# Performance work log

Measured on AMD Instinct MI355X. Metric: run time of the kernel, lower is better.

The kernel has to match this reference:

```python
import jax, jax.numpy as jnp
import numpy as np

PARTITIONS = [1, 2, 4, 8, 16, 32]
FORECAST = 720
D_MODEL = 256
B, C = 64, 64


def len_of_split_into_k_parts(L, k):
    avg, rem = L // k, L % k
    return [avg + (1 if i < rem else 0) for i in range(k)]


def setup_inputs() -> dict:
    key = jax.random.key(0)
    keys = jax.random.split(key, 1 + 2 * len(PARTITIONS))
    T = sum(PARTITIONS)
    inp = {"x": jax.random.normal(keys[0], (B, C, T, D_MODEL), dtype=jnp.float32)}
    for i, k in enumerate(PARTITIONS):
        max_len = max(len_of_split_into_k_parts(FORECAST, k))
        bound = 1.0 / np.sqrt(D_MODEL)
        inp[f"W{i}"] = jax.random.uniform(keys[1 + 2 * i], (max_len, D_MODEL), minval=-bound, maxval=bound, dtype=jnp.float32)
        inp[f"b{i}"] = jax.random.uniform(keys[2 + 2 * i], (max_len,), minval=-bound, maxval=bound, dtype=jnp.float32)
    return inp


def _forward(x, Ws, bs):
    idx = 0
    total = None
    for i, k in enumerate(PARTITIONS):
        split = len_of_split_into_k_parts(FORECAST, k)
        x_r = x[..., idx:idx + k, :]                      # [B, C, k, d]
        idx += k
        proj = jnp.einsum('bctd,md->bctm', x_r, Ws[i]) + bs[i]  # [B, C, k, max_len]
        # ragged slice+concat: token s contributes its first split[s] positions
        tok = np.repeat(np.arange(k), split)              # [f] static indices
        pos = np.concatenate([np.arange(s) for s in split])  # [f]
        res = proj[..., tok, pos]                         # [B, C, f]
        total = res if total is None else total + res
    return jnp.swapaxes(total, -1, -2)                    # [B, f, C]


def reference(x, W0, b0, W1, b1, W2, b2, W3, b3, W4, b4, W5, b5):
    Ws = [W0, W1, W2, W3, W4, W5]
    bs = [b0, b1, b2, b3, b4, b5]
    return _forward(x, Ws, bs)
```

## Files before the change

### kernel.cpp

```cpp
#include <hip/hip_runtime.h>
#include <stdint.h>


#define FDIM 720
#define DDIM 256
#define TDIM 63
#define NSUBTOT 299
#define TAB_BYTES ((size_t)NSUBTOT * 8 * 1024)
#define OUTELEMS ((size_t)64 * FDIM * 64)
#define NCHUNK 80
#define CH 6

typedef __attribute__((ext_vector_type(8))) short short8;
typedef __attribute__((ext_vector_type(4))) float f32x4;

__device__ __forceinline__ uint32_t pkru(float a, float b) {
    uint32_t ua = __builtin_bit_cast(uint32_t, a) + 0x8000u;
    uint32_t ub = __builtin_bit_cast(uint32_t, b) + 0x8000u;
    return __builtin_amdgcn_perm(ub, ua, 0x07060302u);
}
__device__ __forceinline__ short8 loadpack(const float* p) {
    float4 v0 = *(const float4*)p;
    float4 v1 = *(const float4*)(p + 4);
    uint4 u;
    u.x = pkru(v0.x, v0.y);
    u.y = pkru(v0.z, v0.w);
    u.z = pkru(v1.x, v1.y);
    u.w = pkru(v1.z, v1.w);
    return __builtin_bit_cast(short8, u);
}

__device__ __forceinline__ void atomAddF(float* p, float v) {
    unsafeAtomicAdd(p, v);
}

__device__ __forceinline__ void jpos(int i, int f, int& j, int& pos) {
    switch (i) {
        case 0: j = 0;       pos = f;            break;
        case 1: j = f / 360; pos = f - 360 * j;  break;
        case 2: j = f / 180; pos = f - 180 * j;  break;
        case 3: j = f / 90;  pos = f - 90 * j;   break;
        case 4: j = f / 45;  pos = f - 45 * j;   break;
        default:
            if (f < 368) { j = f / 23;  pos = f - 23 * j; }
            else { int g = f - 368; int q = g / 22; j = 16 + q; pos = g - 22 * q; }
            break;
    }
}

__device__ __forceinline__ void tok_params(int tok, int& len, int& ns,
                                           int& start, int& tabsub) {
    if (tok < 1)       { len = 720; ns = 45; start = 0;
                         tabsub = 0; }
    else if (tok < 3)  { int j = tok - 1;  len = 360; ns = 23; start = 360 * j;
                         tabsub = 45 + j * 23; }
    else if (tok < 7)  { int j = tok - 3;  len = 180; ns = 12; start = 180 * j;
                         tabsub = 91 + j * 12; }
    else if (tok < 15) { int j = tok - 7;  len = 90;  ns = 6;  start = 90 * j;
                         tabsub = 139 + j * 6; }
    else if (tok < 31) { int j = tok - 15; len = 45;  ns = 3;  start = 45 * j;
                         tabsub = 187 + j * 3; }
    else               { int j = tok - 31;
                         len = (j < 16) ? 23 : 22;
                         start = (j < 16) ? 23 * j : 368 + 22 * (j - 16);
                         ns = 2; tabsub = 235 + j * 2; }
}

__device__ __forceinline__ void chunk_params(int cid, int& tok, int& s0) {
    if (cid < 8)       { tok = 0;               s0 = CH * cid; }
    else if (cid < 16) { int q = cid - 8;  tok = 1 + (q >> 2); s0 = CH * (q & 3); }
    else if (cid < 24) { int q = cid - 16; tok = 3 + (q >> 1); s0 = CH * (q & 1); }
    else if (cid < 32) { tok = 7 + (cid - 24);  s0 = 0; }
    else if (cid < 48) { tok = 15 + (cid - 32); s0 = 0; }
    else               { tok = 31 + (cid - 48); s0 = 0; }
}

__global__ __launch_bounds__(256) void olrs_prep(
    const float* __restrict__ W0, const float* __restrict__ W1,
    const float* __restrict__ W2, const float* __restrict__ W3,
    const float* __restrict__ W4, const float* __restrict__ W5,
    char* __restrict__ ws)
{
    const int gid  = blockIdx.x * 256 + threadIdx.x;
    const int lane = gid & 63;
    const int fid  = gid >> 6;
    if (fid >= NSUBTOT * 8) return;
    const int ks = fid & 7;
    const int g  = fid >> 3;

    int len; const float* W;
    int s;
    if (g < 45)       { W = W0; len = 720; s = g; }
    else if (g < 91)  { int g2 = g - 45;  W = W1; len = 360; s = g2 % 23; }
    else if (g < 139) { int g2 = g - 91;  W = W2; len = 180; s = g2 % 12; }
    else if (g < 187) { int g2 = g - 139; W = W3; len = 90;  s = g2 % 6; }
    else if (g < 235) { int g2 = g - 187; W = W4; len = 45;  s = g2 % 3; }
    else              { int g2 = g - 235; W = W5; int j = g2 >> 1;
                        len = (j < 16) ? 23 : 22; s = g2 & 1; }

    const int m15  = lane & 15;
    const int koct = lane >> 4;
    const int pos  = s * 16 + m15;
    uint4 u = {0u, 0u, 0u, 0u};
    if (pos < len) {
        const float* src = W + (size_t)pos * DDIM + ks * 32 + koct * 8;
        float4 v0 = *(const float4*)src;
        float4 v1 = *(const float4*)(src + 4);
        u.x = pkru(v0.x, v0.y);
        u.y = pkru(v0.z, v0.w);
        u.z = pkru(v1.x, v1.y);
        u.w = pkru(v1.z, v1.w);
    }
    *(uint4*)(ws + (size_t)fid * 1024 + lane * 16) = u;
}

__global__ __launch_bounds__(256) void olrs_init(
    const float* __restrict__ b0, const float* __restrict__ b1,
    const float* __restrict__ b2, const float* __restrict__ b3,
    const float* __restrict__ b4, const float* __restrict__ b5,
    float* __restrict__ out)
{
    const size_t base = ((size_t)blockIdx.x * 256 + threadIdx.x) * 4;
    if (base >= OUTELEMS) return;
    const int f = (int)((base >> 6) % FDIM);
    int j, p;
    float s = b0[f];
    jpos(1, f, j, p); s += b1[p];
    jpos(2, f, j, p); s += b2[p];
    jpos(3, f, j, p); s += b3[p];
    jpos(4, f, j, p); s += b4[p];
    jpos(5, f, j, p); s += b5[p];
    float4 o = {s, s, s, s};
    *(float4*)(out + base) = o;
}

__global__ __launch_bounds__(256) void olrs_main_at(
    const float* __restrict__ x,
    const char* __restrict__ ws,
    float* __restrict__ out)
{
    const int wid   = blockIdx.x * 4 + (threadIdx.x >> 6);
    const int lane  = threadIdx.x & 63;
    const int cid   = wid >> 7;
    const int ntile = wid & 127;
    const int b     = ntile >> 1;
    const int c0    = (ntile & 1) << 5;
    const int m15   = lane & 15;
    const int koct  = lane >> 4;

    int tok, s0;
    chunk_params(cid, tok, s0);
    int len, ns, start, tabsub;
    tok_params(tok, len, ns, start, tabsub);
    const int send = (s0 + CH < ns) ? (s0 + CH) : ns;

    const float* xpl = x + (((size_t)(b * 64 + c0 + m15)) * TDIM + tok) * DDIM;
    const float* xph = xpl + (size_t)16 * TDIM * DDIM;
    short8 xl[8], xh[8];
    #pragma unroll
    for (int ks = 0; ks < 8; ks++)
        xl[ks] = loadpack(xpl + ks * 32 + koct * 8);
    #pragma unroll
    for (int ks = 0; ks < 8; ks++)
        xh[ks] = loadpack(xph + ks * 32 + koct * 8);

    const char* tab = ws + (size_t)tabsub * 8192 + lane * 16;
    float* obl = out + ((size_t)b * FDIM + start) * 64 + c0 + m15;
    float* obh = obl + 16;

    short8 wA[8], wB[8];

    auto loadW = [&](short8* w, int s) {
        const char* t = tab + (size_t)s * 8192;
        #pragma unroll
        for (int ks = 0; ks < 8; ks++)
            w[ks] = *(const short8*)(t + ks * 1024);
    };
    auto compute = [&](const short8* w, int s) {
        f32x4 al0 = {0.f, 0.f, 0.f, 0.f}, al1 = {0.f, 0.f, 0.f, 0.f};
        f32x4 ah0 = {0.f, 0.f, 0.f, 0.f}, ah1 = {0.f, 0.f, 0.f, 0.f};
        #pragma unroll
        for (int ks = 0; ks < 8; ks += 2) {
            al0 = __builtin_amdgcn_mfma_f32_16x16x32_bf16(w[ks],     xl[ks],     al0, 0, 0, 0);
            ah0 = __builtin_amdgcn_mfma_f32_16x16x32_bf16(w[ks],     xh[ks],     ah0, 0, 0, 0);
            al1 = __builtin_amdgcn_mfma_f32_16x16x32_bf16(w[ks + 1], xl[ks + 1], al1, 0, 0, 0);
            ah1 = __builtin_amdgcn_mfma_f32_16x16x32_bf16(w[ks + 1], xh[ks + 1], ah1, 0, 0, 0);
        }
        const int fl0 = s * 16 + koct * 4;
        #pragma unroll
        for (int rg = 0; rg < 4; rg++) {
            const int fl = fl0 + rg;
            if (fl < len) {
                atomAddF(obl + (size_t)fl * 64, al0[rg] + al1[rg]);
                atomAddF(obh + (size_t)fl * 64, ah0[rg] + ah1[rg]);
            }
        }
    };

    int s = s0;
    loadW(wA, s);
    for (;;) {
        if (s + 1 < send) loadW(wB, s + 1);
        compute(wA, s);
        if (++s >= send) break;
        if (s + 1 < send) loadW(wA, s + 1);
        compute(wB, s);
        if (++s >= send) break;
    }
}

__device__ __forceinline__ int startf(int i, int j) {
    switch (i) {
        case 0: return 0;
        case 1: return 360 * j;
        case 2: return 180 * j;
        case 3: return 90 * j;
        case 4: return 45 * j;
        default: return (j < 16) ? 23 * j : 368 + 22 * (j - 16);
    }
}

__global__ __launch_bounds__(256) void olrs_fb(
    const float* __restrict__ x,
    const float* __restrict__ W0, const float* __restrict__ b0,
    const float* __restrict__ W1, const float* __restrict__ b1,
    const float* __restrict__ W2, const float* __restrict__ b2,
    const float* __restrict__ W3, const float* __restrict__ b3,
    const float* __restrict__ W4, const float* __restrict__ b4,
    const float* __restrict__ W5, const float* __restrict__ b5,
    float* __restrict__ out)
{
    const float* Wp[6] = {W0, W1, W2, W3, W4, W5};
    const float* bp[6] = {b0, b1, b2, b3, b4, b5};
    const int TB[6] = {0, 1, 3, 7, 15, 31};

    const int wid  = blockIdx.x * 4 + (threadIdx.x >> 6);
    const int lane = threadIdx.x & 63;
    const int ft   = wid % 45;
    const int bc   = wid / 45;
    const int b    = bc >> 2;
    const int c0   = (bc & 3) << 4;
    const int f0   = ft << 4;
    const int m15  = lane & 15;
    const int koct = lane >> 4;
    const size_t xrow = (size_t)(b * 64 + c0 + m15) * TDIM;

    f32x4 acc = {0.f, 0.f, 0.f, 0.f};
    #pragma unroll
    for (int i = 0; i < 6; i++) {
        int jlo, plo, jhi, phi;
        jpos(i, f0, jlo, plo);
        jpos(i, f0 + 15, jhi, phi);
        const bool cross = (jhi > jlo);
        const int fb = cross ? (startf(i, jhi) - f0) : 16;
        const float* xlo = x + (xrow + TB[i] + jlo) * DDIM;
        const float* xhi = x + (xrow + TB[i] + jhi) * DDIM;
        int jw, pw;
        jpos(i, f0 + m15, jw, pw);
        const float* wsrc = Wp[i] + (size_t)pw * DDIM;
        #pragma unroll
        for (int ks = 0; ks < 8; ks++) {
            const int d0 = ks * 32 + koct * 8;
            short8 a = loadpack(wsrc + d0);
            short8 blo = loadpack(xlo + d0);
            if (!cross) {
                acc = __builtin_amdgcn_mfma_f32_16x16x32_bf16(a, blo, acc, 0, 0, 0);
            } else {
                short8 bhi = loadpack(xhi + d0);
                short8 z;
                #pragma unroll
                for (int q = 0; q < 8; q++) z[q] = 0;
                short8 alo = (m15 < fb) ? a : z;
                short8 ahi = (m15 < fb) ? z : a;
                acc = __builtin_amdgcn_mfma_f32_16x16x32_bf16(alo, blo, acc, 0, 0, 0);
                acc = __builtin_amdgcn_mfma_f32_16x16x32_bf16(ahi, bhi, acc, 0, 0, 0);
            }
        }
    }
    #pragma unroll
    for (int rg = 0; rg < 4; rg++) {
        const int f = f0 + koct * 4 + rg;
        float bias = 0.f;
        #pragma unroll
        for (int i = 0; i < 6; i++) {
            int j, pos;
            jpos(i, f, j, pos);
            bias += bp[i][pos];
        }
        out[((size_t)b * FDIM + f) * 64 + c0 + m15] = acc[rg] + bias;
    }
}

extern "C" void kernel_launch(void* const* d_in, const int* in_sizes, int n_in,
                              void* d_out, int out_size, void* d_ws, size_t ws_size,
                              hipStream_t stream) {
    (void)in_sizes; (void)n_in; (void)out_size;

    const float* x  = (const float*)d_in[0];
    const float* W0 = (const float*)d_in[1];
    const float* b0 = (const float*)d_in[2];
    const float* W1 = (const float*)d_in[3];
    const float* b1 = (const float*)d_in[4];
    const float* W2 = (const float*)d_in[5];
    const float* b2 = (const float*)d_in[6];
    const float* W3 = (const float*)d_in[7];
    const float* b3 = (const float*)d_in[8];
    const float* W4 = (const float*)d_in[9];
    const float* b4 = (const float*)d_in[10];
    const float* W5 = (const float*)d_in[11];
    const float* b5 = (const float*)d_in[12];
    float* out = (float*)d_out;

    if (ws_size >= TAB_BYTES) {
        char* ws = (char*)d_ws;
        olrs_prep<<<dim3(NSUBTOT * 8 * 64 / 256), dim3(256), 0, stream>>>(
            W0, W1, W2, W3, W4, W5, ws);
        olrs_init<<<dim3((unsigned)(OUTELEMS / 4 / 256)), dim3(256), 0, stream>>>(
            b0, b1, b2, b3, b4, b5, out);
        olrs_main_at<<<dim3(NCHUNK * 128 / 4), dim3(256), 0, stream>>>(x, ws, out);
    } else {
        olrs_fb<<<dim3(45 * 256), dim3(256), 0, stream>>>(
            x, W0, b0, W1, b1, W2, b2, W3, b3, W4, b4, W5, b5, out);
    }
}
```

Before: 91.66 us.

## Merge prep/init kernels and share bf16 x tiles through LDS across waves

Fuses the weight-table packing kernel and the bias-initialisation kernel into one launch, removing a kernel launch and its gap. The main kernel now assigns the four waves of a block to chunks of the same token (or paired tokens), so the block loads and converts each x tile to bf16 once, stages it in LDS in MFMA fragment order, and every wave reads it from there. Before, each wave re-read and re-converted the same x data from global memory. This adds a block barrier and 32 KB of LDS per block, which may reduce occupancy.

```diff
diff --git a/kernel.cpp b/kernel.cpp
--- a/kernel.cpp
+++ b/kernel.cpp
@@ -8,8 +8,7 @@
 #define NSUBTOT 299
 #define TAB_BYTES ((size_t)NSUBTOT * 8 * 1024)
 #define OUTELEMS ((size_t)64 * FDIM * 64)
-#define NCHUNK 80
-#define CH 6
+#define NPREPTHR (NSUBTOT * 8 * 64)
 
 typedef __attribute__((ext_vector_type(8))) short short8;
 typedef __attribute__((ext_vector_type(4))) float f32x4;
@@ -66,103 +65,133 @@
                          ns = 2; tabsub = 235 + j * 2; }
 }
 
-__device__ __forceinline__ void chunk_params(int cid, int& tok, int& s0) {
-    if (cid < 8)       { tok = 0;               s0 = CH * cid; }
-    else if (cid < 16) { int q = cid - 8;  tok = 1 + (q >> 2); s0 = CH * (q & 3); }
-    else if (cid < 24) { int q = cid - 16; tok = 3 + (q >> 1); s0 = CH * (q & 1); }
-    else if (cid < 32) { tok = 7 + (cid - 24);  s0 = 0; }
-    else if (cid < 48) { tok = 15 + (cid - 32); s0 = 0; }
-    else               { tok = 31 + (cid - 48); s0 = 0; }
-}
-
-__global__ __launch_bounds__(256) void olrs_prep(
+__global__ __launch_bounds__(256) void olrs_prepinit(
     const float* __restrict__ W0, const float* __restrict__ W1,
     const float* __restrict__ W2, const float* __restrict__ W3,
     const float* __restrict__ W4, const float* __restrict__ W5,
-    char* __restrict__ ws)
-{
-    const int gid  = blockIdx.x * 256 + threadIdx.x;
-    const int lane = gid & 63;
-    const int fid  = gid >> 6;
-    if (fid >= NSUBTOT * 8) return;
-    const int ks = fid & 7;
-    const int g  = fid >> 3;
-
-    int len; const float* W;
-    int s;
-    if (g < 45)       { W = W0; len = 720; s = g; }
-    else if (g < 91)  { int g2 = g - 45;  W = W1; len = 360; s = g2 % 23; }
-    else if (g < 139) { int g2 = g - 91;  W = W2; len = 180; s = g2 % 12; }
-    else if (g < 187) { int g2 = g - 139; W = W3; len = 90;  s = g2 % 6; }
-    else if (g < 235) { int g2 = g - 187; W = W4; len = 45;  s = g2 % 3; }
-    else              { int g2 = g - 235; W = W5; int j = g2 >> 1;
-                        len = (j < 16) ? 23 : 22; s = g2 & 1; }
-
-    const int m15  = lane & 15;
-    const int koct = lane >> 4;
-    const int pos  = s * 16 + m15;
-    uint4 u = {0u, 0u, 0u, 0u};
-    if (pos < len) {
-        const float* src = W + (size_t)pos * DDIM + ks * 32 + koct * 8;
-        float4 v0 = *(const float4*)src;
-        float4 v1 = *(const float4*)(src + 4);
-        u.x = pkru(v0.x, v0.y);
-        u.y = pkru(v0.z, v0.w);
-        u.z = pkru(v1.x, v1.y);
-        u.w = pkru(v1.z, v1.w);
-    }
-    *(uint4*)(ws + (size_t)fid * 1024 + lane * 16) = u;
-}
-
-__global__ __launch_bounds__(256) void olrs_init(
     const float* __restrict__ b0, const float* __restrict__ b1,
     const float* __restrict__ b2, const float* __restrict__ b3,
     const float* __restrict__ b4, const float* __restrict__ b5,
-    float* __restrict__ out)
+    char* __restrict__ ws, float* __restrict__ out)
 {
-    const size_t base = ((size_t)blockIdx.x * 256 + threadIdx.x) * 4;
-    if (base >= OUTELEMS) return;
-    const int f = (int)((base >> 6) % FDIM);
-    int j, p;
-    float s = b0[f];
-    jpos(1, f, j, p); s += b1[p];
-    jpos(2, f, j, p); s += b2[p];
-    jpos(3, f, j, p); s += b3[p];
-    jpos(4, f, j, p); s += b4[p];
-    jpos(5, f, j, p); s += b5[p];
-    float4 o = {s, s, s, s};
-    *(float4*)(out + base) = o;
-}
-
-__global__ __launch_bounds__(256) void olrs_main_at(
+    const int gid = blockIdx.x * 256 + threadIdx.x;
+
+    const size_t base = (size_t)gid * 4;
+    if (base < OUTELEMS) {
+        const int f = (int)((base >> 6) % FDIM);
+        int j, p;
+        float s = b0[f];
+        jpos(1, f, j, p); s += b1[p];
+        jpos(2, f, j, p); s += b2[p];
+        jpos(3, f, j, p); s += b3[p];
+        jpos(4, f, j, p); s += b4[p];
+        jpos(5, f, j, p); s += b5[p];
+        float4 o = {s, s, s, s};
+        *(float4*)(out + base) = o;
+    }
+
+    if (gid < NPREPTHR) {
+        const int lane = gid & 63;
+        const int fid  = gid >> 6;
+        const int ks = fid & 7;
+        const int g  = fid >> 3;
+
+        int len; const float* W; int s;
+        if (g < 45)       { W = W0; len = 720; s = g; }
+        else if (g < 91)  { int g2 = g - 45;  W = W1; len = 360; s = g2 % 23; }
+        else if (g < 139) { int g2 = g - 91;  W = W2; len = 180; s = g2 % 12; }
+        else if (g < 187) { int g2 = g - 139; W = W3; len = 90;  s = g2 % 6; }
+        else if (g < 235) { int g2 = g - 187; W = W4; len = 45;  s = g2 % 3; }
+        else              { int g2 = g - 235; W = W5; int j = g2 >> 1;
+                            len = (j < 16) ? 23 : 22; s = g2 & 1; }
+
+        const int m15  = lane & 15;
+        const int koct = lane >> 4;
+        const int pos  = s * 16 + m15;
+        uint4 u = {0u, 0u, 0u, 0u};
+        if (pos < len) {
+            const float* src = W + (size_t)pos * DDIM + ks * 32 + koct * 8;
+            float4 v0 = *(const float4*)src;
+            float4 v1 = *(const float4*)(src + 4);
+            u.x = pkru(v0.x, v0.y);
+            u.y = pkru(v0.z, v0.w);
+            u.z = pkru(v1.x, v1.y);
+            u.w = pkru(v1.z, v1.w);
+        }
+        *(uint4*)(ws + (size_t)fid * 1024 + lane * 16) = u;
+    }
+}
+
+__global__ __launch_bounds__(256) void olrs_main8(
     const float* __restrict__ x,
     const char* __restrict__ ws,
     float* __restrict__ out)
 {
-    const int wid   = blockIdx.x * 4 + (threadIdx.x >> 6);
+    __shared__ char lds[32768];
+
+    const int bid   = blockIdx.x;
+    const int rid   = bid >> 7;
+    const int ntile = bid & 127;
+    const int w     = threadIdx.x >> 6;
     const int lane  = threadIdx.x & 63;
-    const int cid   = wid >> 7;
-    const int ntile = wid & 127;
     const int b     = ntile >> 1;
     const int c0    = (ntile & 1) << 5;
     const int m15   = lane & 15;
     const int koct  = lane >> 4;
 
-    int tok, s0;
-    chunk_params(cid, tok, s0);
+    int tok, s0, slab;
+    bool shx;
+    if (rid < 2)      { tok = 0;            s0 = rid * 24 + w * 6; shx = true;  slab = 0; }
+    else if (rid < 4) { tok = rid - 1;      s0 = w * 6;            shx = true;  slab = 0; }
+    else if (rid < 6) { int tb = 3 + (rid - 4) * 2;
+                        tok = tb + (w >> 1); s0 = (w & 1) * 6;     shx = true;  slab = w >> 1; }
+    else              { tok = 7 + (rid - 6) * 4 + w; s0 = 0;       shx = false; slab = 0; }
+
     int len, ns, start, tabsub;
     tok_params(tok, len, ns, start, tabsub);
-    const int send = (s0 + CH < ns) ? (s0 + CH) : ns;
-
-    const float* xpl = x + (((size_t)(b * 64 + c0 + m15)) * TDIM + tok) * DDIM;
-    const float* xph = xpl + (size_t)16 * TDIM * DDIM;
+    const int send = (s0 + 6 < ns) ? (s0 + 6) : ns;
+
     short8 xl[8], xh[8];
-    #pragma unroll
-    for (int ks = 0; ks < 8; ks++)
-        xl[ks] = loadpack(xpl + ks * 32 + koct * 8);
-    #pragma unroll
-    for (int ks = 0; ks < 8; ks++)
-        xh[ks] = loadpack(xph + ks * 32 + koct * 8);
+    if (shx) {
+        const int nslab   = (rid >= 4 && rid < 6) ? 2 : 1;
+        const int tokbase = (rid < 2) ? 0 : ((rid < 4) ? (rid - 1) : 3 + (rid - 4) * 2);
+        const int cc = threadIdx.x >> 3;
+        const int t8 = threadIdx.x & 7;
+        for (int sl = 0; sl < nslab; sl++) {
+            const float* src = x + (((size_t)(b * 64 + c0 + cc)) * TDIM + tokbase + sl) * DDIM;
+            char* dst = lds + sl * 16384;
+            #pragma unroll
+            for (int rep = 0; rep < 4; rep++) {
+                const int d8 = t8 + rep * 8;
+                float4 v0 = *(const float4*)(src + d8 * 8);
+                float4 v1 = *(const float4*)(src + d8 * 8 + 4);
+                uint4 u;
+                u.x = pkru(v0.x, v0.y);
+                u.y = pkru(v0.z, v0.w);
+                u.z = pkru(v1.x, v1.y);
+                u.w = pkru(v1.z, v1.w);
+                const int slot = ((d8 >> 2) * 2 + (cc >> 4)) * 64
+                               + (d8 & 3) * 16 + (cc & 15);
+                *(uint4*)(dst + slot * 16) = u;
+            }
+        }
+        __syncthreads();
+        const char* sb = lds + slab * 16384;
+        #pragma unroll
+        for (int ks = 0; ks < 8; ks++) {
+            xl[ks] = *(const short8*)(sb + ((ks * 2 + 0) * 64 + lane) * 16);
+            xh[ks] = *(const short8*)(sb + ((ks * 2 + 1) * 64 + lane) * 16);
+        }
+    } else {
+        const float* xpl = x + (((size_t)(b * 64 + c0 + m15)) * TDIM + tok) * DDIM;
+        const float* xph = xpl + (size_t)16 * TDIM * DDIM;
+        #pragma unroll
+        for (int ks = 0; ks < 8; ks++)
+            xl[ks] = loadpack(xpl + ks * 32 + koct * 8);
+        #pragma unroll
+        for (int ks = 0; ks < 8; ks++)
+            xh[ks] = loadpack(xph + ks * 32 + koct * 8);
+    }
 
     const char* tab = ws + (size_t)tabsub * 8192 + lane * 16;
     float* obl = out + ((size_t)b * FDIM + start) * 64 + c0 + m15;
@@ -170,21 +199,21 @@
 
     short8 wA[8], wB[8];
 
-    auto loadW = [&](short8* w, int s) {
+    auto loadW = [&](short8* wreg, int s) {
         const char* t = tab + (size_t)s * 8192;
         #pragma unroll
         for (int ks = 0; ks < 8; ks++)
-            w[ks] = *(const short8*)(t + ks * 1024);
+            wreg[ks] = *(const short8*)(t + ks * 1024);
     };
-    auto compute = [&](const short8* w, int s) {
+    auto compute = [&](const short8* wreg, int s) {
         f32x4 al0 = {0.f, 0.f, 0.f, 0.f}, al1 = {0.f, 0.f, 0.f, 0.f};
         f32x4 ah0 = {0.f, 0.f, 0.f, 0.f}, ah1 = {0.f, 0.f, 0.f, 0.f};
         #pragma unroll
         for (int ks = 0; ks < 8; ks += 2) {
-            al0 = __builtin_amdgcn_mfma_f32_16x16x32_bf16(w[ks],     xl[ks],     al0, 0, 0, 0);
-            ah0 = __builtin_amdgcn_mfma_f32_16x16x32_bf16(w[ks],     xh[ks],     ah0, 0, 0, 0);
-            al1 = __builtin_amdgcn_mfma_f32_16x16x32_bf16(w[ks + 1], xl[ks + 1], al1, 0, 0, 0);
-            ah1 = __builtin_amdgcn_mfma_f32_16x16x32_bf16(w[ks + 1], xh[ks + 1], ah1, 0, 0, 0);
+            al0 = __builtin_amdgcn_mfma_f32_16x16x32_bf16(wreg[ks],     xl[ks],     al0, 0, 0, 0);
+            ah0 = __builtin_amdgcn_mfma_f32_16x16x32_bf16(wreg[ks],     xh[ks],     ah0, 0, 0, 0);
+            al1 = __builtin_amdgcn_mfma_f32_16x16x32_bf16(wreg[ks + 1], xl[ks + 1], al1, 0, 0, 0);
+            ah1 = __builtin_amdgcn_mfma_f32_16x16x32_bf16(wreg[ks + 1], xh[ks + 1], ah1, 0, 0, 0);
         }
         const int fl0 = s * 16 + koct * 4;
         #pragma unroll
@@ -313,11 +342,9 @@
 
     if (ws_size >= TAB_BYTES) {
         char* ws = (char*)d_ws;
-        olrs_prep<<<dim3(NSUBTOT * 8 * 64 / 256), dim3(256), 0, stream>>>(
-            W0, W1, W2, W3, W4, W5, ws);
-        olrs_init<<<dim3((unsigned)(OUTELEMS / 4 / 256)), dim3(256), 0, stream>>>(
-            b0, b1, b2, b3, b4, b5, out);
-        olrs_main_at<<<dim3(NCHUNK * 128 / 4), dim3(256), 0, stream>>>(x, ws, out);
+        olrs_prepinit<<<dim3((unsigned)(OUTELEMS / 4 / 256)), dim3(256), 0, stream>>>(
+            W0, W1, W2, W3, W4, W5, b0, b1, b2, b3, b4, b5, ws, out);
+        olrs_main8<<<dim3(20 * 128), dim3(256), 0, stream>>>(x, ws, out);
     } else {
         olrs_fb<<<dim3(45 * 256), dim3(256), 0, stream>>>(
             x, W0, b0, W1, b1, W2, b2, W3, b3, W4, b4, W5, b5, out);
```

New measurement: 86.93 us. 5.2% less time.
